# Kernel tuning notes

Measured on AMD Instinct MI355X. Metric: run time of the kernel, lower is better.

## Reference

```python
import jax, jax.numpy as jnp
import numpy as np

BSZ, T, H, P, N = 2, 2048, 16, 64, 64

def setup_inputs() -> dict:
    key = jax.random.key(0)
    k1, k2, k3, k4, k5 = jax.random.split(key, 5)
    X = jax.random.normal(k1, (BSZ, T, H, P), dtype=jnp.float32)
    delta = jax.random.uniform(k2, (BSZ, T, H), dtype=jnp.float32)
    Bmat = jax.random.normal(k3, (BSZ, T, N), dtype=jnp.float32)
    Cmat = jax.random.normal(k4, (BSZ, T, N), dtype=jnp.float32)
    # module init: A_log = log(arange(1, n_heads+1))
    A_log = jnp.log(jnp.arange(1, H + 1, dtype=jnp.float32))
    return {"X": X, "delta": delta, "Bmat": Bmat, "Cmat": Cmat, "A_log": A_log}

def reference(X, delta, Bmat, Cmat, A_log):
    # X: [B,T,H,P], delta: [B,T,H], Bmat/Cmat: [B,T,N], A_log: [H]
    Bsz, Tlen, Hh, Pp = X.shape
    Nn = Bmat.shape[-1]
    dA = jnp.exp(delta * -jnp.exp(A_log))  # [B,T,H] per-step scalar decay

    def step(h, inp):
        dA_t, dt_t, X_t, B_t, C_t = inp  # [B,H], [B,H], [B,H,P], [B,N], [B,N]
        # outer-product input: delta * X outer B -> [B,H,P,N]
        dBx = (dt_t[:, :, None, None] * X_t[..., None]) * B_t[:, None, None, :]
        h = dA_t[:, :, None, None] * h + dBx
        y_t = jnp.einsum('bhpn,bn->bhp', h, C_t)
        return h, y_t

    h0 = jnp.zeros((Bsz, Hh, Pp, Nn), dtype=X.dtype)
    xs = (
        jnp.moveaxis(dA, 1, 0),    # [T,B,H]
        jnp.moveaxis(delta, 1, 0), # [T,B,H]
        jnp.moveaxis(X, 1, 0),     # [T,B,H,P]
        jnp.moveaxis(Bmat, 1, 0),  # [T,B,N]
        jnp.moveaxis(Cmat, 1, 0),  # [T,B,N]
    )
    h_last, ys = jax.lax.scan(step, h0, xs)
    y = jnp.moveaxis(ys, 0, 1)  # [B,T,H,P]
    return y, h_last
```

## Files before the change

kernel.cpp:

```cpp
#include <hip/hip_runtime.h>


constexpr int BSZ = 2, T = 2048, H = 16, P = 64, N = 64;
constexpr int L = 64, NC = T / L;
constexpr int LS = 72;

using bf16x8 = __attribute__((ext_vector_type(8))) short;
using f32x4  = __attribute__((ext_vector_type(4))) float;

__device__ inline ushort f2bf(float f) {
    unsigned u = __float_as_uint(f);
    u += 0x7FFFu + ((u >> 16) & 1u);
    return (ushort)(u >> 16);
}
__device__ inline unsigned pack2(float a, float b) {
    return (unsigned)f2bf(a) | ((unsigned)f2bf(b) << 16);
}
__device__ inline float bf2f(ushort h) {
    return __uint_as_float(((unsigned)h) << 16);
}

__global__ __launch_bounds__(256, 4) void k1_hend(
    const float* __restrict__ X, const float* __restrict__ delta,
    const float* __restrict__ Bm, const float* __restrict__ A_log,
    ushort* __restrict__ Hbuf, float* __restrict__ Dchunk)
{
    __shared__ __align__(16) ushort sBt[64 * LS];
    __shared__ __align__(16) ushort sXt[64 * LS];
    __shared__ float sWf[64];

    const int tid  = threadIdx.x, lane = tid & 63, w = tid >> 6;
    const int quad = lane >> 4,   l16  = lane & 15;
    const int blk = blockIdx.x;
    const int h   = blk & (H - 1);
    const int c   = (blk >> 4) & (NC - 1);
    const int b   = blk >> 9;
    const int t0  = c * L;
    const int chunkid = (b * H + h) * NC + c;

    {
        const float* gB = Bm + ((size_t)b * T + t0) * N;
        #pragma unroll
        for (int i = 0; i < 8; ++i) {
            int tau = (w * 8 + i) * 2;
            *(unsigned*)&sBt[lane * LS + tau] =
                pack2(gB[(size_t)tau * N + lane], gB[(size_t)(tau + 1) * N + lane]);
        }
    }
    {
        const float* gX = X + (((size_t)b * T + t0) * H + h) * P;
        #pragma unroll
        for (int i = 0; i < 8; ++i) {
            int tau = w * 16 + 2 * i;
            *(unsigned*)&sXt[lane * LS + tau] =
                pack2(gX[(size_t)tau * (H * P) + lane],
                      gX[(size_t)(tau + 1) * (H * P) + lane]);
        }
    }
    if (w == 0) {
        float dl = delta[((size_t)b * T + t0 + lane) * H + h];
        float s = -__expf(A_log[h]) * dl;
        #pragma unroll
        for (int off = 1; off < 64; off <<= 1) {
            float u = __shfl_up(s, off, 64);
            if (lane >= off) s += u;
        }
        float sL = __shfl(s, 63, 64);
        sWf[lane] = __expf(sL + __logf(dl) - s);
        if (lane == 63) Dchunk[chunkid] = __expf(sL);
    }
    __syncthreads();

    f32x4 ha[4];
    #pragma unroll
    for (int j = 0; j < 4; ++j) ha[j] = (f32x4){0.f, 0.f, 0.f, 0.f};
    #pragma unroll
    for (int ks = 0; ks < 2; ++ks) {
        const int ko = ks * 32 + quad * 8;
        bf16x8 xa = *(const bf16x8*)&sXt[(w * 16 + l16) * LS + ko];
        union { bf16x8 v; unsigned u[4]; } xw;
        #pragma unroll
        for (int j2 = 0; j2 < 4; ++j2)
            xw.u[j2] = pack2(bf2f((ushort)xa[2*j2])   * sWf[ko + 2*j2],
                             bf2f((ushort)xa[2*j2+1]) * sWf[ko + 2*j2+1]);
        #pragma unroll
        for (int jn = 0; jn < 4; ++jn) {
            bf16x8 bb = *(const bf16x8*)&sBt[(jn * 16 + l16) * LS + ko];
            ha[jn] = __builtin_amdgcn_mfma_f32_16x16x32_bf16(xw.v, bb, ha[jn], 0, 0, 0);
        }
    }
    __syncthreads();
    #pragma unroll
    for (int jn = 0; jn < 4; ++jn)
        #pragma unroll
        for (int r = 0; r < 4; ++r)
            sBt[(w * 16 + quad * 4 + r) * LS + jn * 16 + l16] = f2bf(ha[jn][r]);
    __syncthreads();
    ushort* Ht = Hbuf + (size_t)chunkid * 4096;
    #pragma unroll
    for (int i = 0; i < 2; ++i) {
        int j = i * 256 + tid, t = j >> 3, col = (j & 7) * 8;
        *(uint4*)&Ht[j * 8] = *(const uint4*)&sBt[t * LS + col];
    }
}

__global__ __launch_bounds__(256, 4) void k2_scan(
    const float* __restrict__ Dchunk, ushort* __restrict__ Hbuf,
    float* __restrict__ Hlast)
{
    const unsigned gid = blockIdx.x * 256u + threadIdx.x;
    const int bh  = gid >> 11;
    const int rem = gid & 2047;
    unsigned* Hb = (unsigned*)Hbuf;
    unsigned v[NC];
    #pragma unroll
    for (int cc = 0; cc < NC; ++cc)
        v[cc] = Hb[(size_t)(bh * NC + cc) * 2048 + rem];
    float hx = 0.f, hy = 0.f;
    #pragma unroll
    for (int cc = 0; cc < NC; ++cc) {
        const float lo = bf2f((ushort)(v[cc] & 0xffffu));
        const float hi = bf2f((ushort)(v[cc] >> 16));
        v[cc] = pack2(hx, hy);
        const float D = Dchunk[bh * NC + cc];
        hx = D * hx + lo;
        hy = D * hy + hi;
    }
    #pragma unroll
    for (int cc = 0; cc < NC; ++cc)
        Hb[(size_t)(bh * NC + cc) * 2048 + rem] = v[cc];
    ((float2*)Hlast)[gid] = make_float2(hx, hy);
}

__global__ __launch_bounds__(256, 4) void k3_y(
    const float* __restrict__ X, const float* __restrict__ delta,
    const float* __restrict__ Bm, const float* __restrict__ Cm,
    const float* __restrict__ A_log, const ushort* __restrict__ Hbuf,
    float* __restrict__ Y)
{
    __shared__ __align__(16) ushort sB [64 * LS];
    __shared__ __align__(16) ushort sC [64 * LS];
    __shared__ __align__(16) ushort sXt[64 * LS];
    __shared__ float sSa[64], sSb[64], sLam[64];

    const int tid  = threadIdx.x, lane = tid & 63, w = tid >> 6;
    const int quad = lane >> 4,   l16  = lane & 15;
    const int blk = blockIdx.x;
    const int h   = blk & (H - 1);
    const int c   = (blk >> 4) & (NC - 1);
    const int b   = blk >> 9;
    const int t0  = c * L;
    const int chunkid = (b * H + h) * NC + c;

    uint4 hreg[2];
    {
        const uint4* Hg4 = (const uint4*)(Hbuf + (size_t)chunkid * 4096);
        hreg[0] = Hg4[tid];
        hreg[1] = Hg4[256 + tid];
    }
    {
        const float4* gB4 = (const float4*)(Bm + ((size_t)b * T + t0) * N);
        const float4* gC4 = (const float4*)(Cm + ((size_t)b * T + t0) * N);
        #pragma unroll
        for (int r = 0; r < 4; ++r) {
            int idx = r * 256 + tid, t = idx >> 4, n4 = (idx & 15) << 2;
            float4 vb = gB4[idx], vc = gC4[idx];
            *(uint2*)&sB[t * LS + n4] = make_uint2(pack2(vb.x, vb.y), pack2(vb.z, vb.w));
            *(uint2*)&sC[t * LS + n4] = make_uint2(pack2(vc.x, vc.y), pack2(vc.z, vc.w));
        }
    }
    {
        const float* gX = X + (((size_t)b * T + t0) * H + h) * P;
        #pragma unroll
        for (int i = 0; i < 8; ++i) {
            int tau = w * 16 + 2 * i;
            *(unsigned*)&sXt[lane * LS + tau] =
                pack2(gX[(size_t)tau * (H * P) + lane],
                      gX[(size_t)(tau + 1) * (H * P) + lane]);
        }
    }
    if (w == 0) {
        float dl = delta[((size_t)b * T + t0 + lane) * H + h];
        float s = -__expf(A_log[h]) * dl;
        #pragma unroll
        for (int off = 1; off < 64; off <<= 1) {
            float u = __shfl_up(s, off, 64);
            if (lane >= off) s += u;
        }
        sSa[lane]  = s;
        sSb[lane]  = __logf(dl) - s;
        sLam[lane] = __expf(s);
    }
    __syncthreads();

    f32x4 g[4];
    #pragma unroll
    for (int j = 0; j < 4; ++j) g[j] = (f32x4){0.f, 0.f, 0.f, 0.f};
    #pragma unroll
    for (int ks = 0; ks < 2; ++ks) {
        const int ko = ks * 32 + quad * 8;
        bf16x8 af = *(const bf16x8*)&sC[(w * 16 + l16) * LS + ko];
        #pragma unroll
        for (int jt = 0; jt < 4; ++jt) {
            bf16x8 bfr = *(const bf16x8*)&sB[(jt * 16 + l16) * LS + ko];
            g[jt] = __builtin_amdgcn_mfma_f32_16x16x32_bf16(af, bfr, g[jt], 0, 0, 0);
        }
    }
    __syncthreads();

    #pragma unroll
    for (int jt = 0; jt < 4; ++jt) {
        const int tau = jt * 16 + l16;
        const float sbv = sSb[tau];
        #pragma unroll
        for (int r = 0; r < 4; ++r) {
            const int t = w * 16 + quad * 4 + r;
            float arg = (tau <= t) ? (sSa[t] + sbv) : -80.0f;
            sB[t * LS + tau] = f2bf(__expf(arg) * g[jt][r]);
        }
    }
    __syncthreads();

    f32x4 ya[4];
    #pragma unroll
    for (int j = 0; j < 4; ++j) ya[j] = (f32x4){0.f, 0.f, 0.f, 0.f};
    #pragma unroll
    for (int ks = 0; ks < 2; ++ks) {
        const int ko = ks * 32 + quad * 8;
        bf16x8 sa = *(const bf16x8*)&sB[(w * 16 + l16) * LS + ko];
        #pragma unroll
        for (int jp = 0; jp < 4; ++jp) {
            bf16x8 xb = *(const bf16x8*)&sXt[(jp * 16 + l16) * LS + ko];
            ya[jp] = __builtin_amdgcn_mfma_f32_16x16x32_bf16(sa, xb, ya[jp], 0, 0, 0);
        }
    }
    __syncthreads();

    #pragma unroll
    for (int i = 0; i < 2; ++i) {
        int j = i * 256 + tid, t = j >> 3, col = (j & 7) * 8;
        *(uint4*)&sXt[t * LS + col] = hreg[i];
    }
    __syncthreads();

    f32x4 acc[4];
    #pragma unroll
    for (int j = 0; j < 4; ++j) acc[j] = (f32x4){0.f, 0.f, 0.f, 0.f};
    #pragma unroll
    for (int ks = 0; ks < 2; ++ks) {
        const int ko = ks * 32 + quad * 8;
        bf16x8 ca = *(const bf16x8*)&sC[(w * 16 + l16) * LS + ko];
        #pragma unroll
        for (int jp = 0; jp < 4; ++jp) {
            bf16x8 hb = *(const bf16x8*)&sXt[(jp * 16 + l16) * LS + ko];
            acc[jp] = __builtin_amdgcn_mfma_f32_16x16x32_bf16(ca, hb, acc[jp], 0, 0, 0);
        }
    }

    float* Yg = Y + (((size_t)b * T + t0) * H + h) * P;
    #pragma unroll
    for (int jp = 0; jp < 4; ++jp)
        #pragma unroll
        for (int r = 0; r < 4; ++r) {
            const int t = w * 16 + quad * 4 + r;
            Yg[(size_t)t * (H * P) + jp * 16 + l16] =
                ya[jp][r] + sLam[t] * acc[jp][r];
        }
}

extern "C" void kernel_launch(void* const* d_in, const int* in_sizes, int n_in,
                              void* d_out, int out_size, void* d_ws, size_t ws_size,
                              hipStream_t stream) {
    const float* X     = (const float*)d_in[0];
    const float* delta = (const float*)d_in[1];
    const float* Bm    = (const float*)d_in[2];
    const float* Cm    = (const float*)d_in[3];
    const float* A_log = (const float*)d_in[4];

    float* Y     = (float*)d_out;
    float* Hlast = (float*)d_out + (size_t)BSZ * T * H * P;

    constexpr size_t TILE = 4096;
    constexpr size_t NTILE = (size_t)BSZ * H * NC;
    ushort* Hbuf  = (ushort*)d_ws;
    float* Dchunk = (float*)((char*)d_ws + NTILE * TILE * sizeof(ushort));

    const int nblk = BSZ * NC * H;
    k1_hend<<<nblk, 256, 0, stream>>>(X, delta, Bm, A_log, Hbuf, Dchunk);
    k2_scan<<<(BSZ * H * P * N / 2) / 256, 256, 0, stream>>>(Dchunk, Hbuf, Hlast);
    k3_y<<<nblk, 256, 0, stream>>>(X, delta, Bm, Cm, A_log, Hbuf, Y);
}
```

Measured before the change: 99.55 us.

## Precompute bf16 swizzled tiles in prep kernel and DMA them into LDS in k3

The first kernel now also writes bf16 copies of the X-transpose, B and C tiles in an XOR-swizzled layout, plus per-chunk cumulative-decay vectors, to workspace. k3 then loads these with global_load_lds direct-to-LDS transfers instead of re-reading fp32 inputs, converting, and redoing the scan. The two output MMAs are merged into one loop, removing barriers. Hbuf and the Hlast indexing are adapted to the swizzled layout. The cost is extra workspace traffic (writing and re-reading bf16 tiles) and more LDS in k3.

```diff
diff --git a/kernel.cpp b/kernel.cpp
--- a/kernel.cpp
+++ b/kernel.cpp
@@ -3,7 +3,7 @@
 
 constexpr int BSZ = 2, T = 2048, H = 16, P = 64, N = 64;
 constexpr int L = 64, NC = T / L;
-constexpr int LS = 72;
+constexpr int LSB = 72;
 
 using bf16x8 = __attribute__((ext_vector_type(8))) short;
 using f32x4  = __attribute__((ext_vector_type(4))) float;
@@ -19,14 +19,29 @@
 __device__ inline float bf2f(ushort h) {
     return __uint_as_float(((unsigned)h) << 16);
 }
-
-__global__ __launch_bounds__(256, 4) void k1_hend(
+__device__ inline int swz(int row, int col) {
+    return row * 64 + ((((col >> 3) ^ (row & 7))) << 3) + (col & 7);
+}
+
+typedef __attribute__((address_space(3))) unsigned int       lds_u32;
+typedef const __attribute__((address_space(1))) unsigned int glb_u32;
+__device__ inline void dma16(const void* g, void* l) {
+    __builtin_amdgcn_global_load_lds((glb_u32*)g, (lds_u32*)l, 16, 0, 0);
+}
+__device__ inline void dma4(const void* g, void* l) {
+    __builtin_amdgcn_global_load_lds((glb_u32*)g, (lds_u32*)l, 4, 0, 0);
+}
+
+__global__ __launch_bounds__(256, 4) void ka_prep(
     const float* __restrict__ X, const float* __restrict__ delta,
-    const float* __restrict__ Bm, const float* __restrict__ A_log,
-    ushort* __restrict__ Hbuf, float* __restrict__ Dchunk)
+    const float* __restrict__ Bm, const float* __restrict__ Cm,
+    const float* __restrict__ A_log,
+    ushort* __restrict__ Xtg, ushort* __restrict__ Hbuf,
+    ushort* __restrict__ Bbf, ushort* __restrict__ Cbf,
+    float* __restrict__ Vec, float* __restrict__ Dchunk)
 {
-    __shared__ __align__(16) ushort sBt[64 * LS];
-    __shared__ __align__(16) ushort sXt[64 * LS];
+    __shared__ __align__(16) ushort sXt[4096];
+    __shared__ __align__(16) ushort sBt[64 * LSB];
     __shared__ float sWf[64];
 
     const int tid  = threadIdx.x, lane = tid & 63, w = tid >> 6;
@@ -37,13 +52,14 @@
     const int b   = blk >> 9;
     const int t0  = c * L;
     const int chunkid = (b * H + h) * NC + c;
+    const int bcid    = b * NC + c;
 
     {
         const float* gB = Bm + ((size_t)b * T + t0) * N;
         #pragma unroll
         for (int i = 0; i < 8; ++i) {
             int tau = (w * 8 + i) * 2;
-            *(unsigned*)&sBt[lane * LS + tau] =
+            *(unsigned*)&sBt[lane * LSB + tau] =
                 pack2(gB[(size_t)tau * N + lane], gB[(size_t)(tau + 1) * N + lane]);
         }
     }
@@ -52,9 +68,24 @@
         #pragma unroll
         for (int i = 0; i < 8; ++i) {
             int tau = w * 16 + 2 * i;
-            *(unsigned*)&sXt[lane * LS + tau] =
+            *(unsigned*)&sXt[swz(lane, tau)] =
                 pack2(gX[(size_t)tau * (H * P) + lane],
                       gX[(size_t)(tau + 1) * (H * P) + lane]);
+        }
+    }
+    if (h == 0) {
+        const float4* gB4 = (const float4*)(Bm + ((size_t)b * T + t0) * N);
+        const float4* gC4 = (const float4*)(Cm + ((size_t)b * T + t0) * N);
+        ushort* Bt = Bbf + (size_t)bcid * 4096;
+        ushort* Ct = Cbf + (size_t)bcid * 4096;
+        #pragma unroll
+        for (int r = 0; r < 4; ++r) {
+            int idx = r * 256 + tid, t = idx >> 4, n4 = idx & 15;
+            int g = n4 >> 1, half = n4 & 1;
+            int off = t * 64 + (((g ^ (t & 7))) << 3) + half * 4;
+            float4 vb = gB4[idx], vc = gC4[idx];
+            *(uint2*)&Bt[off] = make_uint2(pack2(vb.x, vb.y), pack2(vb.z, vb.w));
+            *(uint2*)&Ct[off] = make_uint2(pack2(vc.x, vc.y), pack2(vc.z, vc.w));
         }
     }
     if (w == 0) {
@@ -65,8 +96,13 @@
             float u = __shfl_up(s, off, 64);
             if (lane >= off) s += u;
         }
-        float sL = __shfl(s, 63, 64);
-        sWf[lane] = __expf(sL + __logf(dl) - s);
+        float sL  = __shfl(s, 63, 64);
+        float lnd = __logf(dl);
+        sWf[lane] = __expf(sL + lnd - s);
+        float* vp = Vec + (size_t)chunkid * 192;
+        vp[lane]       = s;
+        vp[64 + lane]  = lnd - s;
+        vp[128 + lane] = __expf(s);
         if (lane == 63) Dchunk[chunkid] = __expf(sL);
     }
     __syncthreads();
@@ -77,7 +113,8 @@
     #pragma unroll
     for (int ks = 0; ks < 2; ++ks) {
         const int ko = ks * 32 + quad * 8;
-        bf16x8 xa = *(const bf16x8*)&sXt[(w * 16 + l16) * LS + ko];
+        const int sg = (ko >> 3) ^ (l16 & 7);
+        bf16x8 xa = *(const bf16x8*)&sXt[(w * 16 + l16) * 64 + sg * 8];
         union { bf16x8 v; unsigned u[4]; } xw;
         #pragma unroll
         for (int j2 = 0; j2 < 4; ++j2)
@@ -85,22 +122,36 @@
                              bf2f((ushort)xa[2*j2+1]) * sWf[ko + 2*j2+1]);
         #pragma unroll
         for (int jn = 0; jn < 4; ++jn) {
-            bf16x8 bb = *(const bf16x8*)&sBt[(jn * 16 + l16) * LS + ko];
+            bf16x8 bb = *(const bf16x8*)&sBt[(jn * 16 + l16) * LSB + ko];
             ha[jn] = __builtin_amdgcn_mfma_f32_16x16x32_bf16(xw.v, bb, ha[jn], 0, 0, 0);
         }
     }
-    __syncthreads();
-    #pragma unroll
-    for (int jn = 0; jn < 4; ++jn)
-        #pragma unroll
-        for (int r = 0; r < 4; ++r)
-            sBt[(w * 16 + quad * 4 + r) * LS + jn * 16 + l16] = f2bf(ha[jn][r]);
-    __syncthreads();
-    ushort* Ht = Hbuf + (size_t)chunkid * 4096;
-    #pragma unroll
-    for (int i = 0; i < 2; ++i) {
-        int j = i * 256 + tid, t = j >> 3, col = (j & 7) * 8;
-        *(uint4*)&Ht[j * 8] = *(const uint4*)&sBt[t * LS + col];
+
+    {
+        ushort* Xtt = Xtg + (size_t)chunkid * 4096;
+        #pragma unroll
+        for (int i = 0; i < 2; ++i) {
+            int j = i * 256 + tid;
+            ((uint4*)Xtt)[j] = ((const uint4*)sXt)[j];
+        }
+    }
+    __syncthreads();
+    {
+        ushort* hst = sBt;
+        #pragma unroll
+        for (int jn = 0; jn < 4; ++jn)
+            #pragma unroll
+            for (int r = 0; r < 4; ++r)
+                hst[swz(w * 16 + quad * 4 + r, jn * 16 + l16)] = f2bf(ha[jn][r]);
+    }
+    __syncthreads();
+    {
+        ushort* Ht = Hbuf + (size_t)chunkid * 4096;
+        #pragma unroll
+        for (int i = 0; i < 2; ++i) {
+            int j = i * 256 + tid;
+            ((uint4*)Ht)[j] = ((const uint4*)sBt)[j];
+        }
     }
 }
 
@@ -129,19 +180,22 @@
     #pragma unroll
     for (int cc = 0; cc < NC; ++cc)
         Hb[(size_t)(bh * NC + cc) * 2048 + rem] = v[cc];
-    ((float2*)Hlast)[gid] = make_float2(hx, hy);
+    const int p   = rem >> 5, w32 = rem & 31;
+    const int g   = (w32 >> 2) ^ (p & 7);
+    const int n0  = (g << 3) + ((w32 & 3) << 1);
+    *(float2*)&Hlast[(size_t)bh * 4096 + p * 64 + n0] = make_float2(hx, hy);
 }
 
 __global__ __launch_bounds__(256, 4) void k3_y(
-    const float* __restrict__ X, const float* __restrict__ delta,
-    const float* __restrict__ Bm, const float* __restrict__ Cm,
-    const float* __restrict__ A_log, const ushort* __restrict__ Hbuf,
-    float* __restrict__ Y)
+    const ushort* __restrict__ Xtg, const ushort* __restrict__ Bbf,
+    const ushort* __restrict__ Cbf, const float* __restrict__ Vec,
+    const ushort* __restrict__ Hbuf, float* __restrict__ Y)
 {
-    __shared__ __align__(16) ushort sB [64 * LS];
-    __shared__ __align__(16) ushort sC [64 * LS];
-    __shared__ __align__(16) ushort sXt[64 * LS];
-    __shared__ float sSa[64], sSb[64], sLam[64];
+    __shared__ __align__(16) ushort sC [4096];
+    __shared__ __align__(16) ushort sB [4096];
+    __shared__ __align__(16) ushort sXt[4096];
+    __shared__ __align__(16) ushort sH [4096];
+    __shared__ float sVec[192];
 
     const int tid  = threadIdx.x, lane = tid & 63, w = tid >> 6;
     const int quad = lane >> 4,   l16  = lane & 15;
@@ -151,59 +205,40 @@
     const int b   = blk >> 9;
     const int t0  = c * L;
     const int chunkid = (b * H + h) * NC + c;
-
-    uint4 hreg[2];
-    {
-        const uint4* Hg4 = (const uint4*)(Hbuf + (size_t)chunkid * 4096);
-        hreg[0] = Hg4[tid];
-        hreg[1] = Hg4[256 + tid];
-    }
-    {
-        const float4* gB4 = (const float4*)(Bm + ((size_t)b * T + t0) * N);
-        const float4* gC4 = (const float4*)(Cm + ((size_t)b * T + t0) * N);
-        #pragma unroll
-        for (int r = 0; r < 4; ++r) {
-            int idx = r * 256 + tid, t = idx >> 4, n4 = (idx & 15) << 2;
-            float4 vb = gB4[idx], vc = gC4[idx];
-            *(uint2*)&sB[t * LS + n4] = make_uint2(pack2(vb.x, vb.y), pack2(vb.z, vb.w));
-            *(uint2*)&sC[t * LS + n4] = make_uint2(pack2(vc.x, vc.y), pack2(vc.z, vc.w));
-        }
-    }
-    {
-        const float* gX = X + (((size_t)b * T + t0) * H + h) * P;
-        #pragma unroll
-        for (int i = 0; i < 8; ++i) {
-            int tau = w * 16 + 2 * i;
-            *(unsigned*)&sXt[lane * LS + tau] =
-                pack2(gX[(size_t)tau * (H * P) + lane],
-                      gX[(size_t)(tau + 1) * (H * P) + lane]);
-        }
-    }
-    if (w == 0) {
-        float dl = delta[((size_t)b * T + t0 + lane) * H + h];
-        float s = -__expf(A_log[h]) * dl;
-        #pragma unroll
-        for (int off = 1; off < 64; off <<= 1) {
-            float u = __shfl_up(s, off, 64);
-            if (lane >= off) s += u;
-        }
-        sSa[lane]  = s;
-        sSb[lane]  = __logf(dl) - s;
-        sLam[lane] = __expf(s);
-    }
-    __syncthreads();
-
-    f32x4 g[4];
-    #pragma unroll
-    for (int j = 0; j < 4; ++j) g[j] = (f32x4){0.f, 0.f, 0.f, 0.f};
+    const int bcid    = b * NC + c;
+
+    {
+        const ushort* gsrc;
+        ushort* ldst;
+        if      (w == 0) { gsrc = Cbf + (size_t)bcid * 4096;    ldst = sC;  }
+        else if (w == 1) { gsrc = Bbf + (size_t)bcid * 4096;    ldst = sB;  }
+        else if (w == 2) { gsrc = Xtg + (size_t)chunkid * 4096; ldst = sXt; }
+        else             { gsrc = Hbuf + (size_t)chunkid * 4096; ldst = sH; }
+        const char* g = (const char*)gsrc + lane * 16;
+        #pragma unroll
+        for (int i = 0; i < 8; ++i)
+            dma16(g + i * 1024, (char*)ldst + i * 1024);
+        if (w == 0) {
+            const float* vp = Vec + (size_t)chunkid * 192;
+            dma4(vp + lane,       sVec);
+            dma4(vp + 64 + lane,  sVec + 64);
+            dma4(vp + 128 + lane, sVec + 128);
+        }
+    }
+    __syncthreads();
+
+    f32x4 g4[4];
+    #pragma unroll
+    for (int j = 0; j < 4; ++j) g4[j] = (f32x4){0.f, 0.f, 0.f, 0.f};
     #pragma unroll
     for (int ks = 0; ks < 2; ++ks) {
         const int ko = ks * 32 + quad * 8;
-        bf16x8 af = *(const bf16x8*)&sC[(w * 16 + l16) * LS + ko];
+        const int sg = (ko >> 3) ^ (l16 & 7);
+        bf16x8 af = *(const bf16x8*)&sC[(w * 16 + l16) * 64 + sg * 8];
         #pragma unroll
         for (int jt = 0; jt < 4; ++jt) {
-            bf16x8 bfr = *(const bf16x8*)&sB[(jt * 16 + l16) * LS + ko];
-            g[jt] = __builtin_amdgcn_mfma_f32_16x16x32_bf16(af, bfr, g[jt], 0, 0, 0);
+            bf16x8 bfr = *(const bf16x8*)&sB[(jt * 16 + l16) * 64 + sg * 8];
+            g4[jt] = __builtin_amdgcn_mfma_f32_16x16x32_bf16(af, bfr, g4[jt], 0, 0, 0);
         }
     }
     __syncthreads();
@@ -211,48 +246,33 @@
     #pragma unroll
     for (int jt = 0; jt < 4; ++jt) {
         const int tau = jt * 16 + l16;
-        const float sbv = sSb[tau];
+        const float sbv = sVec[64 + tau];
         #pragma unroll
         for (int r = 0; r < 4; ++r) {
             const int t = w * 16 + quad * 4 + r;
-            float arg = (tau <= t) ? (sSa[t] + sbv) : -80.0f;
-            sB[t * LS + tau] = f2bf(__expf(arg) * g[jt][r]);
-        }
-    }
-    __syncthreads();
-
-    f32x4 ya[4];
-    #pragma unroll
-    for (int j = 0; j < 4; ++j) ya[j] = (f32x4){0.f, 0.f, 0.f, 0.f};
+            float arg = (tau <= t) ? (sVec[t] + sbv) : -80.0f;
+            sB[swz(t, tau)] = f2bf(__expf(arg) * g4[jt][r]);
+        }
+    }
+    __syncthreads();
+
+    f32x4 ya[4], acc[4];
+    #pragma unroll
+    for (int j = 0; j < 4; ++j) {
+        ya[j]  = (f32x4){0.f, 0.f, 0.f, 0.f};
+        acc[j] = (f32x4){0.f, 0.f, 0.f, 0.f};
+    }
     #pragma unroll
     for (int ks = 0; ks < 2; ++ks) {
         const int ko = ks * 32 + quad * 8;
-        bf16x8 sa = *(const bf16x8*)&sB[(w * 16 + l16) * LS + ko];
+        const int sg = (ko >> 3) ^ (l16 & 7);
+        bf16x8 sa = *(const bf16x8*)&sB[(w * 16 + l16) * 64 + sg * 8];
+        bf16x8 ca = *(const bf16x8*)&sC[(w * 16 + l16) * 64 + sg * 8];
         #pragma unroll
         for (int jp = 0; jp < 4; ++jp) {
-            bf16x8 xb = *(const bf16x8*)&sXt[(jp * 16 + l16) * LS + ko];
-            ya[jp] = __builtin_amdgcn_mfma_f32_16x16x32_bf16(sa, xb, ya[jp], 0, 0, 0);
-        }
-    }
-    __syncthreads();
-
-    #pragma unroll
-    for (int i = 0; i < 2; ++i) {
-        int j = i * 256 + tid, t = j >> 3, col = (j & 7) * 8;
-        *(uint4*)&sXt[t * LS + col] = hreg[i];
-    }
-    __syncthreads();
-
-    f32x4 acc[4];
-    #pragma unroll
-    for (int j = 0; j < 4; ++j) acc[j] = (f32x4){0.f, 0.f, 0.f, 0.f};
-    #pragma unroll
-    for (int ks = 0; ks < 2; ++ks) {
-        const int ko = ks * 32 + quad * 8;
-        bf16x8 ca = *(const bf16x8*)&sC[(w * 16 + l16) * LS + ko];
-        #pragma unroll
-        for (int jp = 0; jp < 4; ++jp) {
-            bf16x8 hb = *(const bf16x8*)&sXt[(jp * 16 + l16) * LS + ko];
+            bf16x8 xb = *(const bf16x8*)&sXt[(jp * 16 + l16) * 64 + sg * 8];
+            bf16x8 hb = *(const bf16x8*)&sH [(jp * 16 + l16) * 64 + sg * 8];
+            ya[jp]  = __builtin_amdgcn_mfma_f32_16x16x32_bf16(sa, xb, ya[jp], 0, 0, 0);
             acc[jp] = __builtin_amdgcn_mfma_f32_16x16x32_bf16(ca, hb, acc[jp], 0, 0, 0);
         }
     }
@@ -264,7 +284,7 @@
         for (int r = 0; r < 4; ++r) {
             const int t = w * 16 + quad * 4 + r;
             Yg[(size_t)t * (H * P) + jp * 16 + l16] =
-                ya[jp][r] + sLam[t] * acc[jp][r];
+                ya[jp][r] + sVec[128 + t] * acc[jp][r];
         }
 }
 
@@ -280,13 +300,17 @@
     float* Y     = (float*)d_out;
     float* Hlast = (float*)d_out + (size_t)BSZ * T * H * P;
 
-    constexpr size_t TILE = 4096;
-    constexpr size_t NTILE = (size_t)BSZ * H * NC;
-    ushort* Hbuf  = (ushort*)d_ws;
-    float* Dchunk = (float*)((char*)d_ws + NTILE * TILE * sizeof(ushort));
+    char* ws = (char*)d_ws;
+    ushort* Hbuf = (ushort*)(ws);
+    ushort* Xtg  = (ushort*)(ws + (8u << 20));
+    ushort* Bbf  = (ushort*)(ws + (16u << 20));
+    ushort* Cbf  = (ushort*)(ws + (16u << 20) + (512u << 10));
+    float*  Vec  = (float*)(ws + (17u << 20));
+    float*  Dchunk = (float*)(ws + (18u << 20));
 
     const int nblk = BSZ * NC * H;
-    k1_hend<<<nblk, 256, 0, stream>>>(X, delta, Bm, A_log, Hbuf, Dchunk);
-    k2_scan<<<(BSZ * H * P * N / 2) / 256, 256, 0, stream>>>(Dchunk, Hbuf, Hlast);
-    k3_y<<<nblk, 256, 0, stream>>>(X, delta, Bm, Cm, A_log, Hbuf, Y);
-}
+    ka_prep<<<nblk, 256, 0, stream>>>(X, delta, Bm, Cm, A_log,
+                                      Xtg, Hbuf, Bbf, Cbf, Vec, Dchunk);
+    k2_scan<<<256, 256, 0, stream>>>(Dchunk, Hbuf, Hlast);
+    k3_y<<<nblk, 256, 0, stream>>>(Xtg, Bbf, Cbf, Vec, Hbuf, Y);
+}
```

Measured after the change: 95.55 us. 4.0% less time.

## Fuse three SSD kernels into one with atomic last-block chunk scan

Applied to the files above, without the earlier changes.

Merges the chunk-state, inter-chunk scan and output kernels into a single launch. The last block to finish for each (batch, head) runs the sequential scan over chunk states, then releases a Done flag that the other blocks spin-wait on before the state-times-C product. Shared-memory tiles switch from padded rows to an XOR swizzle. This removes two kernel launches and the reload of X/B between kernels, at the cost of spin-waiting blocks that depend on co-residency, a serial scan done by one block per head, and a memset launch.

```diff
diff --git a/kernel.cpp b/kernel.cpp
--- a/kernel.cpp
+++ b/kernel.cpp
@@ -3,7 +3,7 @@
 
 constexpr int BSZ = 2, T = 2048, H = 16, P = 64, N = 64;
 constexpr int L = 64, NC = T / L;
-constexpr int LS = 72;
+constexpr int NBH = BSZ * H;
 
 using bf16x8 = __attribute__((ext_vector_type(8))) short;
 using f32x4  = __attribute__((ext_vector_type(4))) float;
@@ -19,15 +19,26 @@
 __device__ inline float bf2f(ushort h) {
     return __uint_as_float(((unsigned)h) << 16);
 }
-
-__global__ __launch_bounds__(256, 4) void k1_hend(
+__device__ inline int swz(int row, int col) {
+    return row * 64 + ((((col >> 3) ^ (row & 7))) << 3) + (col & 7);
+}
+
+__global__ __launch_bounds__(256, 4) void fused_ssd(
     const float* __restrict__ X, const float* __restrict__ delta,
-    const float* __restrict__ Bm, const float* __restrict__ A_log,
-    ushort* __restrict__ Hbuf, float* __restrict__ Dchunk)
+    const float* __restrict__ Bm, const float* __restrict__ Cm,
+    const float* __restrict__ A_log,
+    float* __restrict__ Y, float* __restrict__ Hlast,
+    ushort* __restrict__ Hbuf,
+    float* __restrict__ Dchunk,
+    int* __restrict__ Ctr,
+    int* __restrict__ Done)
 {
-    __shared__ __align__(16) ushort sBt[64 * LS];
-    __shared__ __align__(16) ushort sXt[64 * LS];
-    __shared__ float sWf[64];
+    __shared__ __align__(16) ushort sC [4096];
+    __shared__ __align__(16) ushort sBn[4096];
+    __shared__ __align__(16) ushort sBt[4096];
+    __shared__ __align__(16) ushort sXt[4096];
+    __shared__ float sSa[64], sSb[64], sLam[64], sWf[64];
+    __shared__ int sOrd;
 
     const int tid  = threadIdx.x, lane = tid & 63, w = tid >> 6;
     const int quad = lane >> 4,   l16  = lane & 15;
@@ -36,23 +47,35 @@
     const int c   = (blk >> 4) & (NC - 1);
     const int b   = blk >> 9;
     const int t0  = c * L;
-    const int chunkid = (b * H + h) * NC + c;
-
+    const int bh  = b * H + h;
+    const int chunkid = bh * NC + c;
+
+    {
+        const float4* gB4 = (const float4*)(Bm + ((size_t)b * T + t0) * N);
+        const float4* gC4 = (const float4*)(Cm + ((size_t)b * T + t0) * N);
+        #pragma unroll
+        for (int r = 0; r < 4; ++r) {
+            int idx = r * 256 + tid, t = idx >> 4, n4 = idx & 15;
+            int g = n4 >> 1, half = n4 & 1;
+            int off = t * 64 + (((g ^ (t & 7))) << 3) + half * 4;
+            float4 vb = gB4[idx], vc = gC4[idx];
+            *(uint2*)&sBn[off] = make_uint2(pack2(vb.x, vb.y), pack2(vb.z, vb.w));
+            *(uint2*)&sC [off] = make_uint2(pack2(vc.x, vc.y), pack2(vc.z, vc.w));
+        }
+    }
     {
         const float* gB = Bm + ((size_t)b * T + t0) * N;
         #pragma unroll
         for (int i = 0; i < 8; ++i) {
             int tau = (w * 8 + i) * 2;
-            *(unsigned*)&sBt[lane * LS + tau] =
+            *(unsigned*)&sBt[swz(lane, tau)] =
                 pack2(gB[(size_t)tau * N + lane], gB[(size_t)(tau + 1) * N + lane]);
         }
-    }
-    {
         const float* gX = X + (((size_t)b * T + t0) * H + h) * P;
         #pragma unroll
         for (int i = 0; i < 8; ++i) {
             int tau = w * 16 + 2 * i;
-            *(unsigned*)&sXt[lane * LS + tau] =
+            *(unsigned*)&sXt[swz(lane, tau)] =
                 pack2(gX[(size_t)tau * (H * P) + lane],
                       gX[(size_t)(tau + 1) * (H * P) + lane]);
         }
@@ -65,8 +88,12 @@
             float u = __shfl_up(s, off, 64);
             if (lane >= off) s += u;
         }
-        float sL = __shfl(s, 63, 64);
-        sWf[lane] = __expf(sL + __logf(dl) - s);
+        float sL  = __shfl(s, 63, 64);
+        float lnd = __logf(dl);
+        sSa[lane]  = s;
+        sSb[lane]  = lnd - s;
+        sLam[lane] = __expf(s);
+        sWf[lane]  = __expf(sL + lnd - s);
         if (lane == 63) Dchunk[chunkid] = __expf(sL);
     }
     __syncthreads();
@@ -77,7 +104,8 @@
     #pragma unroll
     for (int ks = 0; ks < 2; ++ks) {
         const int ko = ks * 32 + quad * 8;
-        bf16x8 xa = *(const bf16x8*)&sXt[(w * 16 + l16) * LS + ko];
+        const int sg = (ko >> 3) ^ (l16 & 7);
+        bf16x8 xa = *(const bf16x8*)&sXt[(w * 16 + l16) * 64 + sg * 8];
         union { bf16x8 v; unsigned u[4]; } xw;
         #pragma unroll
         for (int j2 = 0; j2 < 4; ++j2)
@@ -85,7 +113,7 @@
                              bf2f((ushort)xa[2*j2+1]) * sWf[ko + 2*j2+1]);
         #pragma unroll
         for (int jn = 0; jn < 4; ++jn) {
-            bf16x8 bb = *(const bf16x8*)&sBt[(jn * 16 + l16) * LS + ko];
+            bf16x8 bb = *(const bf16x8*)&sBt[(jn * 16 + l16) * 64 + sg * 8];
             ha[jn] = __builtin_amdgcn_mfma_f32_16x16x32_bf16(xw.v, bb, ha[jn], 0, 0, 0);
         }
     }
@@ -94,116 +122,77 @@
     for (int jn = 0; jn < 4; ++jn)
         #pragma unroll
         for (int r = 0; r < 4; ++r)
-            sBt[(w * 16 + quad * 4 + r) * LS + jn * 16 + l16] = f2bf(ha[jn][r]);
-    __syncthreads();
-    ushort* Ht = Hbuf + (size_t)chunkid * 4096;
-    #pragma unroll
-    for (int i = 0; i < 2; ++i) {
-        int j = i * 256 + tid, t = j >> 3, col = (j & 7) * 8;
-        *(uint4*)&Ht[j * 8] = *(const uint4*)&sBt[t * LS + col];
-    }
-}
-
-__global__ __launch_bounds__(256, 4) void k2_scan(
-    const float* __restrict__ Dchunk, ushort* __restrict__ Hbuf,
-    float* __restrict__ Hlast)
-{
-    const unsigned gid = blockIdx.x * 256u + threadIdx.x;
-    const int bh  = gid >> 11;
-    const int rem = gid & 2047;
-    unsigned* Hb = (unsigned*)Hbuf;
-    unsigned v[NC];
-    #pragma unroll
-    for (int cc = 0; cc < NC; ++cc)
-        v[cc] = Hb[(size_t)(bh * NC + cc) * 2048 + rem];
-    float hx = 0.f, hy = 0.f;
-    #pragma unroll
-    for (int cc = 0; cc < NC; ++cc) {
-        const float lo = bf2f((ushort)(v[cc] & 0xffffu));
-        const float hi = bf2f((ushort)(v[cc] >> 16));
-        v[cc] = pack2(hx, hy);
-        const float D = Dchunk[bh * NC + cc];
-        hx = D * hx + lo;
-        hy = D * hy + hi;
-    }
-    #pragma unroll
-    for (int cc = 0; cc < NC; ++cc)
-        Hb[(size_t)(bh * NC + cc) * 2048 + rem] = v[cc];
-    ((float2*)Hlast)[gid] = make_float2(hx, hy);
-}
-
-__global__ __launch_bounds__(256, 4) void k3_y(
-    const float* __restrict__ X, const float* __restrict__ delta,
-    const float* __restrict__ Bm, const float* __restrict__ Cm,
-    const float* __restrict__ A_log, const ushort* __restrict__ Hbuf,
-    float* __restrict__ Y)
-{
-    __shared__ __align__(16) ushort sB [64 * LS];
-    __shared__ __align__(16) ushort sC [64 * LS];
-    __shared__ __align__(16) ushort sXt[64 * LS];
-    __shared__ float sSa[64], sSb[64], sLam[64];
-
-    const int tid  = threadIdx.x, lane = tid & 63, w = tid >> 6;
-    const int quad = lane >> 4,   l16  = lane & 15;
-    const int blk = blockIdx.x;
-    const int h   = blk & (H - 1);
-    const int c   = (blk >> 4) & (NC - 1);
-    const int b   = blk >> 9;
-    const int t0  = c * L;
-    const int chunkid = (b * H + h) * NC + c;
-
-    uint4 hreg[2];
-    {
-        const uint4* Hg4 = (const uint4*)(Hbuf + (size_t)chunkid * 4096);
-        hreg[0] = Hg4[tid];
-        hreg[1] = Hg4[256 + tid];
-    }
-    {
-        const float4* gB4 = (const float4*)(Bm + ((size_t)b * T + t0) * N);
-        const float4* gC4 = (const float4*)(Cm + ((size_t)b * T + t0) * N);
-        #pragma unroll
-        for (int r = 0; r < 4; ++r) {
-            int idx = r * 256 + tid, t = idx >> 4, n4 = (idx & 15) << 2;
-            float4 vb = gB4[idx], vc = gC4[idx];
-            *(uint2*)&sB[t * LS + n4] = make_uint2(pack2(vb.x, vb.y), pack2(vb.z, vb.w));
-            *(uint2*)&sC[t * LS + n4] = make_uint2(pack2(vc.x, vc.y), pack2(vc.z, vc.w));
-        }
-    }
-    {
-        const float* gX = X + (((size_t)b * T + t0) * H + h) * P;
-        #pragma unroll
-        for (int i = 0; i < 8; ++i) {
-            int tau = w * 16 + 2 * i;
-            *(unsigned*)&sXt[lane * LS + tau] =
-                pack2(gX[(size_t)tau * (H * P) + lane],
-                      gX[(size_t)(tau + 1) * (H * P) + lane]);
-        }
-    }
-    if (w == 0) {
-        float dl = delta[((size_t)b * T + t0 + lane) * H + h];
-        float s = -__expf(A_log[h]) * dl;
-        #pragma unroll
-        for (int off = 1; off < 64; off <<= 1) {
-            float u = __shfl_up(s, off, 64);
-            if (lane >= off) s += u;
-        }
-        sSa[lane]  = s;
-        sSb[lane]  = __logf(dl) - s;
-        sLam[lane] = __expf(s);
-    }
-    __syncthreads();
-
-    f32x4 g[4];
-    #pragma unroll
-    for (int j = 0; j < 4; ++j) g[j] = (f32x4){0.f, 0.f, 0.f, 0.f};
-    #pragma unroll
-    for (int ks = 0; ks < 2; ++ks) {
-        const int ko = ks * 32 + quad * 8;
-        bf16x8 af = *(const bf16x8*)&sC[(w * 16 + l16) * LS + ko];
+            sBt[swz(w * 16 + quad * 4 + r, jn * 16 + l16)] = f2bf(ha[jn][r]);
+    __syncthreads();
+    {
+        ushort* Ht = Hbuf + (size_t)chunkid * 4096;
+        ((uint4*)Ht)[tid]       = ((const uint4*)sBt)[tid];
+        ((uint4*)Ht)[256 + tid] = ((const uint4*)sBt)[256 + tid];
+    }
+    __syncthreads();
+
+    if (tid == 0) {
+        __threadfence();
+        sOrd = __hip_atomic_fetch_add(&Ctr[bh], 1, __ATOMIC_ACQ_REL,
+                                      __HIP_MEMORY_SCOPE_AGENT);
+    }
+    __syncthreads();
+    const bool isScan = (sOrd == NBH - 0 - 1 + (NC - NBH));
+    const bool scanner = (sOrd == NC - 1);
+
+    if (scanner) {
+        unsigned* Hb = (unsigned*)(Hbuf + (size_t)bh * NC * 4096);
+        const float* Dp = Dchunk + bh * NC;
+        float hs[16];
+        #pragma unroll
+        for (int e = 0; e < 16; ++e) hs[e] = 0.f;
+        for (int cc = 0; cc < NC; ++cc) {
+            uint4* tp = (uint4*)(Hb + cc * 2048);
+            uint4 t0v = tp[tid];
+            uint4 t1v = tp[256 + tid];
+            const float D = Dp[cc];
+            uint4 s0, s1;
+            unsigned tin[8] = {t0v.x, t0v.y, t0v.z, t0v.w, t1v.x, t1v.y, t1v.z, t1v.w};
+            unsigned sout[8];
+            #pragma unroll
+            for (int j = 0; j < 8; ++j) {
+                sout[j] = pack2(hs[2*j], hs[2*j+1]);
+                hs[2*j]   = D * hs[2*j]   + bf2f((ushort)(tin[j] & 0xffffu));
+                hs[2*j+1] = D * hs[2*j+1] + bf2f((ushort)(tin[j] >> 16));
+            }
+            s0 = make_uint4(sout[0], sout[1], sout[2], sout[3]);
+            s1 = make_uint4(sout[4], sout[5], sout[6], sout[7]);
+            tp[tid]       = s0;
+            tp[256 + tid] = s1;
+        }
+        #pragma unroll
+        for (int q = 0; q < 2; ++q) {
+            const int u4  = q * 256 + tid;
+            const int row = u4 >> 3;
+            const int rg  = (u4 & 7) ^ (row & 7);
+            float* dst = Hlast + (size_t)bh * 4096 + row * 64 + rg * 8;
+            *(float4*)dst       = make_float4(hs[8*q+0], hs[8*q+1], hs[8*q+2], hs[8*q+3]);
+            *(float4*)(dst + 4) = make_float4(hs[8*q+4], hs[8*q+5], hs[8*q+6], hs[8*q+7]);
+        }
+        if (tid == 0) {
+            __threadfence();
+            __hip_atomic_store(&Done[bh], 1, __ATOMIC_RELEASE,
+                               __HIP_MEMORY_SCOPE_AGENT);
+        }
+    }
+
+    f32x4 g4[4];
+    #pragma unroll
+    for (int j = 0; j < 4; ++j) g4[j] = (f32x4){0.f, 0.f, 0.f, 0.f};
+    #pragma unroll
+    for (int ks = 0; ks < 2; ++ks) {
+        const int ko = ks * 32 + quad * 8;
+        const int sg = (ko >> 3) ^ (l16 & 7);
+        bf16x8 af = *(const bf16x8*)&sC[(w * 16 + l16) * 64 + sg * 8];
         #pragma unroll
         for (int jt = 0; jt < 4; ++jt) {
-            bf16x8 bfr = *(const bf16x8*)&sB[(jt * 16 + l16) * LS + ko];
-            g[jt] = __builtin_amdgcn_mfma_f32_16x16x32_bf16(af, bfr, g[jt], 0, 0, 0);
+            bf16x8 bfr = *(const bf16x8*)&sBn[(jt * 16 + l16) * 64 + sg * 8];
+            g4[jt] = __builtin_amdgcn_mfma_f32_16x16x32_bf16(af, bfr, g4[jt], 0, 0, 0);
         }
     }
     __syncthreads();
@@ -216,7 +205,7 @@
         for (int r = 0; r < 4; ++r) {
             const int t = w * 16 + quad * 4 + r;
             float arg = (tau <= t) ? (sSa[t] + sbv) : -80.0f;
-            sB[t * LS + tau] = f2bf(__expf(arg) * g[jt][r]);
+            sBn[swz(t, tau)] = f2bf(__expf(arg) * g4[jt][r]);
         }
     }
     __syncthreads();
@@ -227,19 +216,27 @@
     #pragma unroll
     for (int ks = 0; ks < 2; ++ks) {
         const int ko = ks * 32 + quad * 8;
-        bf16x8 sa = *(const bf16x8*)&sB[(w * 16 + l16) * LS + ko];
+        const int sg = (ko >> 3) ^ (l16 & 7);
+        bf16x8 sa = *(const bf16x8*)&sBn[(w * 16 + l16) * 64 + sg * 8];
         #pragma unroll
         for (int jp = 0; jp < 4; ++jp) {
-            bf16x8 xb = *(const bf16x8*)&sXt[(jp * 16 + l16) * LS + ko];
+            bf16x8 xb = *(const bf16x8*)&sXt[(jp * 16 + l16) * 64 + sg * 8];
             ya[jp] = __builtin_amdgcn_mfma_f32_16x16x32_bf16(sa, xb, ya[jp], 0, 0, 0);
         }
     }
-    __syncthreads();
-
-    #pragma unroll
-    for (int i = 0; i < 2; ++i) {
-        int j = i * 256 + tid, t = j >> 3, col = (j & 7) * 8;
-        *(uint4*)&sXt[t * LS + col] = hreg[i];
+
+    if (tid == 0) {
+        while (__hip_atomic_load(&Done[bh], __ATOMIC_ACQUIRE,
+                                 __HIP_MEMORY_SCOPE_AGENT) == 0)
+            __builtin_amdgcn_s_sleep(8);
+    }
+    __syncthreads();
+
+    {
+        const uint4* Ht = (const uint4*)(Hbuf + (size_t)chunkid * 4096);
+        uint4 h0 = Ht[tid], h1 = Ht[256 + tid];
+        ((uint4*)sBt)[tid]       = h0;
+        ((uint4*)sBt)[256 + tid] = h1;
     }
     __syncthreads();
 
@@ -249,10 +246,11 @@
     #pragma unroll
     for (int ks = 0; ks < 2; ++ks) {
         const int ko = ks * 32 + quad * 8;
-        bf16x8 ca = *(const bf16x8*)&sC[(w * 16 + l16) * LS + ko];
+        const int sg = (ko >> 3) ^ (l16 & 7);
+        bf16x8 ca = *(const bf16x8*)&sC[(w * 16 + l16) * 64 + sg * 8];
         #pragma unroll
         for (int jp = 0; jp < 4; ++jp) {
-            bf16x8 hb = *(const bf16x8*)&sXt[(jp * 16 + l16) * LS + ko];
+            bf16x8 hb = *(const bf16x8*)&sBt[(jp * 16 + l16) * 64 + sg * 8];
             acc[jp] = __builtin_amdgcn_mfma_f32_16x16x32_bf16(ca, hb, acc[jp], 0, 0, 0);
         }
     }
@@ -266,6 +264,7 @@
             Yg[(size_t)t * (H * P) + jp * 16 + l16] =
                 ya[jp][r] + sLam[t] * acc[jp][r];
         }
+    (void)isScan;
 }
 
 extern "C" void kernel_launch(void* const* d_in, const int* in_sizes, int n_in,
@@ -280,13 +279,14 @@
     float* Y     = (float*)d_out;
     float* Hlast = (float*)d_out + (size_t)BSZ * T * H * P;
 
-    constexpr size_t TILE = 4096;
-    constexpr size_t NTILE = (size_t)BSZ * H * NC;
-    ushort* Hbuf  = (ushort*)d_ws;
-    float* Dchunk = (float*)((char*)d_ws + NTILE * TILE * sizeof(ushort));
-
-    const int nblk = BSZ * NC * H;
-    k1_hend<<<nblk, 256, 0, stream>>>(X, delta, Bm, A_log, Hbuf, Dchunk);
-    k2_scan<<<(BSZ * H * P * N / 2) / 256, 256, 0, stream>>>(Dchunk, Hbuf, Hlast);
-    k3_y<<<nblk, 256, 0, stream>>>(X, delta, Bm, Cm, A_log, Hbuf, Y);
-}
+    char* ws = (char*)d_ws;
+    ushort* Hbuf  = (ushort*)ws;
+    float* Dchunk = (float*)(ws + (8u << 20));
+    int*   Ctr    = (int*)(ws + (8u << 20) + 4096);
+    int*   Done   = (int*)(ws + (8u << 20) + 4096 + 128);
+
+    hipMemsetAsync(Ctr, 0, 256, stream);
+
+    fused_ssd<<<BSZ * NC * H, 256, 0, stream>>>(
+        X, delta, Bm, Cm, A_log, Y, Hlast, Hbuf, Dchunk, Ctr, Done);
+}
```

Result: slower. 358.7 us (+260.3%).
